# Optimization experiments

Measured on AMD Instinct MI355X. Metric: run time of the kernel, lower is better.

## Reference

```python
import jax, jax.numpy as jnp
import numpy as np

T, D, H, E = 8192, 1024, 512, 8
BLK = 32  # MXFP8 scaling block size along the contraction dim


def setup_inputs() -> dict:
    key = jax.random.key(0)
    k1, k2, k3, k4 = jax.random.split(key, 4)
    # qdata: values representable-ish in e4m3 (we use small normal floats)
    output_e4m3 = jax.random.normal(k1, (T, D), dtype=jnp.float32)
    # e8m0 scales are powers of two, one per 32-element block along dim
    output_scales_e8m0 = jnp.exp2(
        jax.random.randint(k2, (T, D // BLK), -2, 3).astype(jnp.float32)
    )
    # uniform token distribution across experts (tokens are expert-contiguous)
    num_tokens_per_expert = jnp.full((E,), T // E, dtype=jnp.int32)
    expert_padded_offsets = jnp.zeros((E,), dtype=jnp.int32)  # unused by forward body
    w13 = jax.random.normal(k3, (E, 2 * H, D), dtype=jnp.float32) * 0.02
    w2 = jax.random.normal(k4, (E, D, H), dtype=jnp.float32) * 0.02
    return {
        "output_e4m3": output_e4m3,
        "output_scales_e8m0": output_scales_e8m0,
        "num_tokens_per_expert": num_tokens_per_expert,
        "expert_padded_offsets": expert_padded_offsets,
        "w13": w13,
        "w2": w2,
    }


def reference(output_e4m3, output_scales_e8m0, num_tokens_per_expert,
              expert_padded_offsets, w13, w2):
    # Dequantize MXFP8: qdata * per-block e8m0 scale, blocks of 32 along dim.
    scales = jnp.repeat(output_scales_e8m0, BLK, axis=-1)  # [T, D]
    x = output_e4m3 * scales  # [T, D] high-precision reference activations
    # Grouped GEMM 1: tokens are expert-contiguous with uniform group sizes,
    # so the ragged grouped matmul reduces to a batched einsum per expert.
    tpe = T // E
    xg = x.reshape(E, tpe, D)                       # [E, tpe, D]
    h13 = jnp.einsum("etd,ehd->eth", xg, w13)       # [E, tpe, 2H]
    h1, h3 = h13[..., :H], h13[..., H:]
    h = jax.nn.silu(h1) * h3                        # fused SiLU-gate
    # Grouped GEMM 2
    out = jnp.einsum("eth,edh->etd", h, w2)         # [E, tpe, D]
    return out.reshape(T, D)
```

## Files before the change

### kernel.cpp

```cpp
#include <hip/hip_runtime.h>
#include <hip/hip_bf16.h>

#define T_TOK 8192
#define DDIM  1024
#define HDIM  512
#define NE    8
#define TPE   (T_TOK / NE)

typedef __attribute__((ext_vector_type(4))) float floatx4;
typedef __attribute__((ext_vector_type(8))) short bf16x8;

__device__ __forceinline__ unsigned short f2bf(float f) {
    union { float f; unsigned int u; } v;
    v.f = f;
    unsigned int u = v.u;
    unsigned int r = u + 0x7FFFu + ((u >> 16) & 1u);
    return (unsigned short)(r >> 16);
}

__device__ __forceinline__ void gld_lds16(const void* g, void* l) {
    __builtin_amdgcn_global_load_lds(
        (const __attribute__((address_space(1))) unsigned int*)g,
        (__attribute__((address_space(3))) unsigned int*)l, 16, 0, 0);
}

__global__ __launch_bounds__(256)
void convert_kernel(const float* __restrict__ X, const float* __restrict__ S,
                    const float* __restrict__ W13, const float* __restrict__ W2,
                    unsigned short* __restrict__ Xb,
                    unsigned short* __restrict__ W13b,
                    unsigned short* __restrict__ W2b)
{
    const int NTX  = (T_TOK * DDIM) / 4;
    const int NT13 = (NE * 2 * HDIM * DDIM) / 4;
    const int NT2  = (NE * DDIM * HDIM) / 4;
    const int stride = gridDim.x * blockDim.x;
    for (int i = blockIdx.x * blockDim.x + threadIdx.x; i < NTX + NT13 + NT2; i += stride) {
        float4 v;
        ushort4* dst;
        if (i < NTX) {
            int row = i >> 8;
            int c4  = i & 255;
            v = reinterpret_cast<const float4*>(X)[i];
            float sc = S[row * (DDIM / 32) + (c4 >> 3)];
            v.x *= sc; v.y *= sc; v.z *= sc; v.w *= sc;
            dst = (ushort4*)Xb + i;
        } else if (i < NTX + NT13) {
            int j = i - NTX;
            v = reinterpret_cast<const float4*>(W13)[j];
            dst = (ushort4*)W13b + j;
        } else {
            int j = i - NTX - NT13;
            v = reinterpret_cast<const float4*>(W2)[j];
            dst = (ushort4*)W2b + j;
        }
        ushort4 b;
        b.x = f2bf(v.x); b.y = f2bf(v.y); b.z = f2bf(v.z); b.w = f2bf(v.w);
        *dst = b;
    }
}

__device__ __forceinline__ int xcd_swizzle_512(int raw) {
    return (raw & 7) * 64 + (raw >> 3);
}

__global__ __launch_bounds__(256, 2)
void gemm1_silu_kernel(const unsigned short* __restrict__ Xb,
                       const unsigned short* __restrict__ W13b,
                       __hip_bfloat16* __restrict__ Hout)
{
    const int bid = xcd_swizzle_512(blockIdx.x);
    const int e  = bid >> 6;
    const int mt = (bid >> 3) & 7;
    const int nt = bid & 7;
    const int tok0 = e * TPE + mt * 128;
    const unsigned short* __restrict__ We = W13b + (size_t)e * (2 * HDIM) * DDIM;

    __shared__ __hip_bfloat16 sA[2][128][64];
    __shared__ __hip_bfloat16 sB[2][128][64];

    const int tid  = threadIdx.x;
    const int lane = tid & 63;
    const int wave = tid >> 6;
    const int wr = wave >> 1;
    const int wc = wave & 1;
    const int lr = lane & 15;
    const int lk = (lane >> 4) * 8;

    floatx4 acc1[4][2] = {};
    floatx4 acc3[4][2] = {};

    const int srow0 = (tid >> 3);
    const int scol  = (tid & 7) * 8;

    auto STAGE = [&](int kk, int buf) {
        const int k0 = kk * 64;
        #pragma unroll
        for (int j = 0; j < 4; ++j) {
            int row = srow0 + j * 32;
            gld_lds16(&Xb[(size_t)(tok0 + row) * DDIM + k0 + scol],
                      &sA[buf][row][scol]);
            int wrow = (j < 2) ? (nt * 64 + row)
                               : (HDIM + nt * 64 + (row - 64));
            gld_lds16(&We[(size_t)wrow * DDIM + k0 + scol],
                      &sB[buf][row][scol]);
        }
    };
    auto COMPUTE = [&](int buf) {
        #pragma unroll
        for (int ks = 0; ks < 2; ++ks) {
            bf16x8 a[4], b1[2], b3[2];
            #pragma unroll
            for (int m = 0; m < 4; ++m)
                a[m] = *reinterpret_cast<const bf16x8*>(&sA[buf][wr * 64 + m * 16 + lr][ks * 32 + lk]);
            #pragma unroll
            for (int n = 0; n < 2; ++n) {
                b1[n] = *reinterpret_cast<const bf16x8*>(&sB[buf][wc * 32 + n * 16 + lr][ks * 32 + lk]);
                b3[n] = *reinterpret_cast<const bf16x8*>(&sB[buf][64 + wc * 32 + n * 16 + lr][ks * 32 + lk]);
            }
            #pragma unroll
            for (int m = 0; m < 4; ++m)
                #pragma unroll
                for (int n = 0; n < 2; ++n) {
                    acc1[m][n] = __builtin_amdgcn_mfma_f32_16x16x32_bf16(a[m], b1[n], acc1[m][n], 0, 0, 0);
                    acc3[m][n] = __builtin_amdgcn_mfma_f32_16x16x32_bf16(a[m], b3[n], acc3[m][n], 0, 0, 0);
                }
        }
    };

    STAGE(0, 0);
    for (int kk = 0; kk < DDIM / 64 - 1; ++kk) {
        STAGE(kk + 1, (kk + 1) & 1);
        asm volatile("s_waitcnt vmcnt(8)" ::: "memory");
        __builtin_amdgcn_sched_barrier(0);
        __builtin_amdgcn_s_barrier();
        COMPUTE(kk & 1);
        __builtin_amdgcn_s_barrier();
    }
    asm volatile("s_waitcnt vmcnt(0)" ::: "memory");
    __builtin_amdgcn_sched_barrier(0);
    __builtin_amdgcn_s_barrier();
    COMPUTE(1);

    const int hcol0 = nt * 64 + wc * 32;
    #pragma unroll
    for (int m = 0; m < 4; ++m) {
        #pragma unroll
        for (int n = 0; n < 2; ++n) {
            #pragma unroll
            for (int i = 0; i < 4; ++i) {
                int row = tok0 + wr * 64 + m * 16 + (lane >> 4) * 4 + i;
                int col = hcol0 + n * 16 + (lane & 15);
                float h1 = acc1[m][n][i];
                float h3 = acc3[m][n][i];
                float sig = 1.0f / (1.0f + __expf(-h1));
                Hout[(size_t)row * HDIM + col] = __float2bfloat16(h1 * sig * h3);
            }
        }
    }
}

__global__ __launch_bounds__(256, 2)
void gemm2_kernel(const __hip_bfloat16* __restrict__ Hin,
                  const unsigned short* __restrict__ W2b,
                  float* __restrict__ Out)
{
    const int bid = xcd_swizzle_512(blockIdx.x);
    const int e  = bid >> 6;
    const int mt = (bid >> 3) & 7;
    const int nt = bid & 7;
    const int tok0 = e * TPE + mt * 128;
    const unsigned short* __restrict__ We = W2b + (size_t)e * DDIM * HDIM;

    __shared__ __hip_bfloat16 sA[2][128][64];
    __shared__ __hip_bfloat16 sB[2][128][64];

    const int tid  = threadIdx.x;
    const int lane = tid & 63;
    const int wave = tid >> 6;
    const int wr = wave >> 1;
    const int wc = wave & 1;
    const int lr = lane & 15;
    const int lk = (lane >> 4) * 8;

    floatx4 acc[4][4] = {};

    const int srow0 = (tid >> 3);
    const int scol  = (tid & 7) * 8;

    auto STAGE = [&](int kk, int buf) {
        const int k0 = kk * 64;
        #pragma unroll
        for (int j = 0; j < 4; ++j) {
            int row = srow0 + j * 32;
            gld_lds16(&Hin[(size_t)(tok0 + row) * HDIM + k0 + scol],
                      &sA[buf][row][scol]);
            gld_lds16(&We[(size_t)(nt * 128 + row) * HDIM + k0 + scol],
                      &sB[buf][row][scol]);
        }
    };
    auto COMPUTE = [&](int buf) {
        #pragma unroll
        for (int ks = 0; ks < 2; ++ks) {
            bf16x8 a[4], b[4];
            #pragma unroll
            for (int m = 0; m < 4; ++m)
                a[m] = *reinterpret_cast<const bf16x8*>(&sA[buf][wr * 64 + m * 16 + lr][ks * 32 + lk]);
            #pragma unroll
            for (int n = 0; n < 4; ++n)
                b[n] = *reinterpret_cast<const bf16x8*>(&sB[buf][wc * 64 + n * 16 + lr][ks * 32 + lk]);
            #pragma unroll
            for (int m = 0; m < 4; ++m)
                #pragma unroll
                for (int n = 0; n < 4; ++n)
                    acc[m][n] = __builtin_amdgcn_mfma_f32_16x16x32_bf16(a[m], b[n], acc[m][n], 0, 0, 0);
        }
    };

    STAGE(0, 0);
    for (int kk = 0; kk < HDIM / 64 - 1; ++kk) {
        STAGE(kk + 1, (kk + 1) & 1);
        asm volatile("s_waitcnt vmcnt(8)" ::: "memory");
        __builtin_amdgcn_sched_barrier(0);
        __builtin_amdgcn_s_barrier();
        COMPUTE(kk & 1);
        __builtin_amdgcn_s_barrier();
    }
    asm volatile("s_waitcnt vmcnt(0)" ::: "memory");
    __builtin_amdgcn_sched_barrier(0);
    __builtin_amdgcn_s_barrier();
    COMPUTE(1);

    const int dcol0 = nt * 128 + wc * 64;
    #pragma unroll
    for (int m = 0; m < 4; ++m) {
        #pragma unroll
        for (int n = 0; n < 4; ++n) {
            #pragma unroll
            for (int i = 0; i < 4; ++i) {
                int row = tok0 + wr * 64 + m * 16 + (lane >> 4) * 4 + i;
                int col = dcol0 + n * 16 + (lane & 15);
                Out[(size_t)row * DDIM + col] = acc[m][n][i];
            }
        }
    }
}

extern "C" void kernel_launch(void* const* d_in, const int* in_sizes, int n_in,
                              void* d_out, int out_size, void* d_ws, size_t ws_size,
                              hipStream_t stream) {
    const float* X   = (const float*)d_in[0];
    const float* S   = (const float*)d_in[1];
    const float* W13 = (const float*)d_in[4];
    const float* W2  = (const float*)d_in[5];
    float* Out = (float*)d_out;

    unsigned short* W13b = (unsigned short*)d_ws;
    unsigned short* W2b  = W13b + (size_t)NE * 2 * HDIM * DDIM;
    __hip_bfloat16* Hb   = (__hip_bfloat16*)(W2b + (size_t)NE * DDIM * HDIM);
    unsigned short* Xb   = (unsigned short*)d_out;

    convert_kernel<<<2048, 256, 0, stream>>>(X, S, W13, W2, Xb, W13b, W2b);
    gemm1_silu_kernel<<<NE * 8 * 8, 256, 0, stream>>>(Xb, W13b, Hb);
    gemm2_kernel<<<NE * 8 * 8, 256, 0, stream>>>(Hb, W2b, Out);
}
```

Measured before the change: 65.55 us.

## Fuse dequant and bf16 conversion into GEMM loads, drop convert kernel

Removes the separate conversion pass. Each GEMM now loads fp32 activations and weights into registers, applies the MXFP8 scale (for X), packs to bf16 with v_cvt_pk_bf16_f32, and writes the result to LDS, using a register-staged double buffer instead of direct global-to-LDS loads. This avoids writing and re-reading the bf16 copies in global memory. In exchange, each block re-reads and re-converts fp32 weights and activations that other tiles also use, which doubles global traffic per tile and adds VALU work and register pressure inside the main loop. The loop also drops one barrier per iteration.

```diff
diff --git a/kernel.cpp b/kernel.cpp
--- a/kernel.cpp
+++ b/kernel.cpp
@@ -10,54 +10,10 @@
 typedef __attribute__((ext_vector_type(4))) float floatx4;
 typedef __attribute__((ext_vector_type(8))) short bf16x8;
 
-__device__ __forceinline__ unsigned short f2bf(float f) {
-    union { float f; unsigned int u; } v;
-    v.f = f;
-    unsigned int u = v.u;
-    unsigned int r = u + 0x7FFFu + ((u >> 16) & 1u);
-    return (unsigned short)(r >> 16);
-}
-
-__device__ __forceinline__ void gld_lds16(const void* g, void* l) {
-    __builtin_amdgcn_global_load_lds(
-        (const __attribute__((address_space(1))) unsigned int*)g,
-        (__attribute__((address_space(3))) unsigned int*)l, 16, 0, 0);
-}
-
-__global__ __launch_bounds__(256)
-void convert_kernel(const float* __restrict__ X, const float* __restrict__ S,
-                    const float* __restrict__ W13, const float* __restrict__ W2,
-                    unsigned short* __restrict__ Xb,
-                    unsigned short* __restrict__ W13b,
-                    unsigned short* __restrict__ W2b)
-{
-    const int NTX  = (T_TOK * DDIM) / 4;
-    const int NT13 = (NE * 2 * HDIM * DDIM) / 4;
-    const int NT2  = (NE * DDIM * HDIM) / 4;
-    const int stride = gridDim.x * blockDim.x;
-    for (int i = blockIdx.x * blockDim.x + threadIdx.x; i < NTX + NT13 + NT2; i += stride) {
-        float4 v;
-        ushort4* dst;
-        if (i < NTX) {
-            int row = i >> 8;
-            int c4  = i & 255;
-            v = reinterpret_cast<const float4*>(X)[i];
-            float sc = S[row * (DDIM / 32) + (c4 >> 3)];
-            v.x *= sc; v.y *= sc; v.z *= sc; v.w *= sc;
-            dst = (ushort4*)Xb + i;
-        } else if (i < NTX + NT13) {
-            int j = i - NTX;
-            v = reinterpret_cast<const float4*>(W13)[j];
-            dst = (ushort4*)W13b + j;
-        } else {
-            int j = i - NTX - NT13;
-            v = reinterpret_cast<const float4*>(W2)[j];
-            dst = (ushort4*)W2b + j;
-        }
-        ushort4 b;
-        b.x = f2bf(v.x); b.y = f2bf(v.y); b.z = f2bf(v.z); b.w = f2bf(v.w);
-        *dst = b;
-    }
+__device__ __forceinline__ unsigned int cvt_pk_bf16(float lo, float hi) {
+    unsigned int r;
+    asm("v_cvt_pk_bf16_f32 %0, %1, %2" : "=v"(r) : "v"(lo), "v"(hi));
+    return r;
 }
 
 __device__ __forceinline__ int xcd_swizzle_512(int raw) {
@@ -65,8 +21,9 @@
 }
 
 __global__ __launch_bounds__(256, 2)
-void gemm1_silu_kernel(const unsigned short* __restrict__ Xb,
-                       const unsigned short* __restrict__ W13b,
+void gemm1_silu_kernel(const float* __restrict__ X,
+                       const float* __restrict__ S,
+                       const float* __restrict__ W13,
                        __hip_bfloat16* __restrict__ Hout)
 {
     const int bid = xcd_swizzle_512(blockIdx.x);
@@ -74,7 +31,7 @@
     const int mt = (bid >> 3) & 7;
     const int nt = bid & 7;
     const int tok0 = e * TPE + mt * 128;
-    const unsigned short* __restrict__ We = W13b + (size_t)e * (2 * HDIM) * DDIM;
+    const float* __restrict__ We = W13 + (size_t)e * (2 * HDIM) * DDIM;
 
     __shared__ __hip_bfloat16 sA[2][128][64];
     __shared__ __hip_bfloat16 sB[2][128][64];
@@ -93,17 +50,41 @@
     const int srow0 = (tid >> 3);
     const int scol  = (tid & 7) * 8;
 
-    auto STAGE = [&](int kk, int buf) {
+    float4 rA[8]; float rs[4]; float4 rB[8];
+
+    auto LOAD = [&](int kk) {
         const int k0 = kk * 64;
         #pragma unroll
         for (int j = 0; j < 4; ++j) {
             int row = srow0 + j * 32;
-            gld_lds16(&Xb[(size_t)(tok0 + row) * DDIM + k0 + scol],
-                      &sA[buf][row][scol]);
+            const float* pa = &X[(size_t)(tok0 + row) * DDIM + k0 + scol];
+            rA[2*j]   = *reinterpret_cast<const float4*>(pa);
+            rA[2*j+1] = *reinterpret_cast<const float4*>(pa + 4);
+            rs[j] = S[(size_t)(tok0 + row) * (DDIM / 32) + ((k0 + scol) >> 5)];
             int wrow = (j < 2) ? (nt * 64 + row)
                                : (HDIM + nt * 64 + (row - 64));
-            gld_lds16(&We[(size_t)wrow * DDIM + k0 + scol],
-                      &sB[buf][row][scol]);
+            const float* pb = &We[(size_t)wrow * DDIM + k0 + scol];
+            rB[2*j]   = *reinterpret_cast<const float4*>(pb);
+            rB[2*j+1] = *reinterpret_cast<const float4*>(pb + 4);
+        }
+    };
+    auto WRITE = [&](int buf) {
+        #pragma unroll
+        for (int j = 0; j < 4; ++j) {
+            int row = srow0 + j * 32;
+            float sc = rs[j];
+            uint4 pa;
+            pa.x = cvt_pk_bf16(rA[2*j].x * sc,   rA[2*j].y * sc);
+            pa.y = cvt_pk_bf16(rA[2*j].z * sc,   rA[2*j].w * sc);
+            pa.z = cvt_pk_bf16(rA[2*j+1].x * sc, rA[2*j+1].y * sc);
+            pa.w = cvt_pk_bf16(rA[2*j+1].z * sc, rA[2*j+1].w * sc);
+            *reinterpret_cast<uint4*>(&sA[buf][row][scol]) = pa;
+            uint4 pb;
+            pb.x = cvt_pk_bf16(rB[2*j].x,   rB[2*j].y);
+            pb.y = cvt_pk_bf16(rB[2*j].z,   rB[2*j].w);
+            pb.z = cvt_pk_bf16(rB[2*j+1].x, rB[2*j+1].y);
+            pb.w = cvt_pk_bf16(rB[2*j+1].z, rB[2*j+1].w);
+            *reinterpret_cast<uint4*>(&sB[buf][row][scol]) = pb;
         }
     };
     auto COMPUTE = [&](int buf) {
@@ -128,19 +109,16 @@
         }
     };
 
-    STAGE(0, 0);
-    for (int kk = 0; kk < DDIM / 64 - 1; ++kk) {
-        STAGE(kk + 1, (kk + 1) & 1);
-        asm volatile("s_waitcnt vmcnt(8)" ::: "memory");
+    LOAD(0);
+    for (int kk = 0; kk < DDIM / 64; ++kk) {
+        const int buf = kk & 1;
+        WRITE(buf);
+        if (kk < DDIM / 64 - 1) LOAD(kk + 1);
+        asm volatile("s_waitcnt lgkmcnt(0)" ::: "memory");
         __builtin_amdgcn_sched_barrier(0);
         __builtin_amdgcn_s_barrier();
-        COMPUTE(kk & 1);
-        __builtin_amdgcn_s_barrier();
-    }
-    asm volatile("s_waitcnt vmcnt(0)" ::: "memory");
-    __builtin_amdgcn_sched_barrier(0);
-    __builtin_amdgcn_s_barrier();
-    COMPUTE(1);
+        COMPUTE(buf);
+    }
 
     const int hcol0 = nt * 64 + wc * 32;
     #pragma unroll
@@ -162,7 +140,7 @@
 
 __global__ __launch_bounds__(256, 2)
 void gemm2_kernel(const __hip_bfloat16* __restrict__ Hin,
-                  const unsigned short* __restrict__ W2b,
+                  const float* __restrict__ W2,
                   float* __restrict__ Out)
 {
     const int bid = xcd_swizzle_512(blockIdx.x);
@@ -170,7 +148,7 @@
     const int mt = (bid >> 3) & 7;
     const int nt = bid & 7;
     const int tok0 = e * TPE + mt * 128;
-    const unsigned short* __restrict__ We = W2b + (size_t)e * DDIM * HDIM;
+    const float* __restrict__ We = W2 + (size_t)e * DDIM * HDIM;
 
     __shared__ __hip_bfloat16 sA[2][128][64];
     __shared__ __hip_bfloat16 sB[2][128][64];
@@ -188,15 +166,31 @@
     const int srow0 = (tid >> 3);
     const int scol  = (tid & 7) * 8;
 
-    auto STAGE = [&](int kk, int buf) {
+    uint4 ra[4]; float4 rB[8];
+
+    auto LOAD = [&](int kk) {
         const int k0 = kk * 64;
         #pragma unroll
         for (int j = 0; j < 4; ++j) {
             int row = srow0 + j * 32;
-            gld_lds16(&Hin[(size_t)(tok0 + row) * HDIM + k0 + scol],
-                      &sA[buf][row][scol]);
-            gld_lds16(&We[(size_t)(nt * 128 + row) * HDIM + k0 + scol],
-                      &sB[buf][row][scol]);
+            ra[j] = *reinterpret_cast<const uint4*>(
+                &Hin[(size_t)(tok0 + row) * HDIM + k0 + scol]);
+            const float* pb = &We[(size_t)(nt * 128 + row) * HDIM + k0 + scol];
+            rB[2*j]   = *reinterpret_cast<const float4*>(pb);
+            rB[2*j+1] = *reinterpret_cast<const float4*>(pb + 4);
+        }
+    };
+    auto WRITE = [&](int buf) {
+        #pragma unroll
+        for (int j = 0; j < 4; ++j) {
+            int row = srow0 + j * 32;
+            *reinterpret_cast<uint4*>(&sA[buf][row][scol]) = ra[j];
+            uint4 pb;
+            pb.x = cvt_pk_bf16(rB[2*j].x,   rB[2*j].y);
+            pb.y = cvt_pk_bf16(rB[2*j].z,   rB[2*j].w);
+            pb.z = cvt_pk_bf16(rB[2*j+1].x, rB[2*j+1].y);
+            pb.w = cvt_pk_bf16(rB[2*j+1].z, rB[2*j+1].w);
+            *reinterpret_cast<uint4*>(&sB[buf][row][scol]) = pb;
         }
     };
     auto COMPUTE = [&](int buf) {
@@ -217,19 +211,16 @@
         }
     };
 
-    STAGE(0, 0);
-    for (int kk = 0; kk < HDIM / 64 - 1; ++kk) {
-        STAGE(kk + 1, (kk + 1) & 1);
-        asm volatile("s_waitcnt vmcnt(8)" ::: "memory");
+    LOAD(0);
+    for (int kk = 0; kk < HDIM / 64; ++kk) {
+        const int buf = kk & 1;
+        WRITE(buf);
+        if (kk < HDIM / 64 - 1) LOAD(kk + 1);
+        asm volatile("s_waitcnt lgkmcnt(0)" ::: "memory");
         __builtin_amdgcn_sched_barrier(0);
         __builtin_amdgcn_s_barrier();
-        COMPUTE(kk & 1);
-        __builtin_amdgcn_s_barrier();
-    }
-    asm volatile("s_waitcnt vmcnt(0)" ::: "memory");
-    __builtin_amdgcn_sched_barrier(0);
-    __builtin_amdgcn_s_barrier();
-    COMPUTE(1);
+        COMPUTE(buf);
+    }
 
     const int dcol0 = nt * 128 + wc * 64;
     #pragma unroll
@@ -255,12 +246,8 @@
     const float* W2  = (const float*)d_in[5];
     float* Out = (float*)d_out;
 
-    unsigned short* W13b = (unsigned short*)d_ws;
-    unsigned short* W2b  = W13b + (size_t)NE * 2 * HDIM * DDIM;
-    __hip_bfloat16* Hb   = (__hip_bfloat16*)(W2b + (size_t)NE * DDIM * HDIM);
-    unsigned short* Xb   = (unsigned short*)d_out;
-
-    convert_kernel<<<2048, 256, 0, stream>>>(X, S, W13, W2, Xb, W13b, W2b);
-    gemm1_silu_kernel<<<NE * 8 * 8, 256, 0, stream>>>(Xb, W13b, Hb);
-    gemm2_kernel<<<NE * 8 * 8, 256, 0, stream>>>(Hb, W2b, Out);
-}
+    __hip_bfloat16* Hb = (__hip_bfloat16*)d_ws;
+
+    gemm1_silu_kernel<<<NE * 8 * 8, 256, 0, stream>>>(X, S, W13, Hb);
+    gemm2_kernel<<<NE * 8 * 8, 256, 0, stream>>>(Hb, W2, Out);
+}
```

After: 86.01 us. +31.2%, slower.
